# Optimization experiments

Measured on AMD Instinct MI355X. Metric: run time of the kernel, lower is better.

Reference implementation:

```python
import jax, jax.numpy as jnp
import numpy as np

VOCAB = 50000
D_EMB = 300
N_BINS = 11
B, LQ, LD = 64, 32, 1024
MU = np.array([1.0, 0.9, 0.7, 0.5, 0.3, 0.1, -0.1, -0.3, -0.5, -0.7, -0.9], dtype=np.float32)
SIGMA = np.array([1e-3] + [0.1] * 10, dtype=np.float32)


def setup_inputs() -> dict:
    key = jax.random.key(0)
    ks = jax.random.split(key, 8)
    inputs_q = jax.random.randint(ks[0], (B, LQ), 0, VOCAB, dtype=jnp.int64 if jax.config.jax_enable_x64 else jnp.int32)
    inputs_d = jax.random.randint(ks[1], (B, LD), 0, VOCAB, dtype=jnp.int64 if jax.config.jax_enable_x64 else jnp.int32)
    mask_q = jnp.ones((B, LQ), dtype=jnp.float32)
    mask_d = jnp.ones((B, LD), dtype=jnp.float32)
    word_emb = jax.random.normal(ks[2], (VOCAB, D_EMB), dtype=jnp.float32) * 0.1
    attn_table = jax.random.uniform(ks[3], (VOCAB, 1), dtype=jnp.float32)  # frozen IDF embedding
    idf_w = jax.random.normal(ks[4], (1, 1), dtype=jnp.float32)
    idf_b = jnp.zeros((1,), dtype=jnp.float32)
    dense_w = jax.random.normal(ks[5], (1, N_BINS), dtype=jnp.float32) * 0.1
    dense_b = jnp.zeros((1,), dtype=jnp.float32)
    return {
        'inputs_q': inputs_q, 'inputs_d': inputs_d,
        'mask_q': mask_q, 'mask_d': mask_d,
        'word_emb': word_emb, 'attn_table': attn_table,
        'idf_w': idf_w, 'idf_b': idf_b,
        'dense_w': dense_w, 'dense_b': dense_b,
    }


def _l2_normalize(x, eps=1e-12):
    # matches F.normalize(x, 2, dim=-1): x / max(||x||, eps)
    n = jnp.sqrt(jnp.sum(x * x, axis=-1, keepdims=True))
    return x / jnp.maximum(n, eps)


def reference(inputs_q, inputs_d, mask_q, mask_d, word_emb, attn_table,
              idf_w, idf_b, dense_w, dense_b):
    mu = jnp.asarray(MU)        # [K]
    sigma = jnp.asarray(SIGMA)  # [K]
    # idf attention on query tokens: Linear(1,1) on frozen embedding lookup
    attn_q = attn_table[inputs_q] * idf_w[0, 0] + idf_b[0]          # [B,Lq,1]
    q_embed = _l2_normalize(word_emb[inputs_q])                      # [B,Lq,E]
    d_embed = _l2_normalize(word_emb[inputs_d])                      # [B,Ld,E]
    sim = jnp.einsum('bqe,bde->bqd', q_embed, d_embed)               # [B,Lq,Ld]
    # RBF soft-histogram over n_bins kernels, doc tokens masked
    rbf = jnp.exp(-((sim[..., None] - mu) ** 2) / (sigma ** 2) / 2)  # [B,Lq,Ld,K]
    pooling_sum = jnp.einsum('bqdk,bd->bqk', rbf, mask_d)            # [B,Lq,K]
    wq = mask_q[..., None] * attn_q                                   # [B,Lq,1]
    log_pool = jnp.log(jnp.clip(pooling_sum, 1e-10)) * wq * 0.01     # [B,Lq,K]
    log_pooling_sum = jnp.sum(log_pool, axis=1)                      # [B,K]
    out = jnp.tanh(log_pooling_sum @ dense_w.T + dense_b)            # [B,1]
    return out[:, 0]                                                 # [B]
```

## Files before the change

kernel.cpp:

```cpp
#include <hip/hip_runtime.h>
#include <math.h>

#define VOCAB  50000
#define D_EMB  300
#define NBINS  11
#define BATCH  64
#define LQ     32
#define LD     1024
#define DTILE  64
#define NDT    (LD / DTILE)
#define NSTEP  10

typedef __attribute__((ext_vector_type(8))) short short8;
typedef __attribute__((ext_vector_type(4))) float floatx4;

__constant__ float c_mu[NBINS]  = {1.0f, 0.9f, 0.7f, 0.5f, 0.3f, 0.1f,
                                   -0.1f, -0.3f, -0.5f, -0.7f, -0.9f};
__constant__ float c_is2[NBINS] = {500000.0f, 50.f, 50.f, 50.f, 50.f, 50.f,
                                   50.f, 50.f, 50.f, 50.f, 50.f};

static __device__ __forceinline__ unsigned short f32_bf16(float f) {
  unsigned u = __float_as_uint(f);
  u += 0x7FFFu + ((u >> 16) & 1u);
  return (unsigned short)(u >> 16);
}
static __device__ __forceinline__ float bf16_f32(unsigned short h) {
  return __uint_as_float(((unsigned)h) << 16);
}

static __device__ __forceinline__ float stage_rows(
    const float* __restrict__ emb_row,
    short* __restrict__ region,
    int s_begin, int s_end, int khi, int lane)
{
  const float4* emb4 = (const float4*)emb_row;
  float p = 0.f;
  for (int s = s_begin; s < s_end; ++s) {
    const int k0 = 32 * s + 8 * khi;
    float4 fa = make_float4(0.f, 0.f, 0.f, 0.f);
    float4 fb = make_float4(0.f, 0.f, 0.f, 0.f);
    if (k0 < D_EMB)     fa = emb4[k0 >> 2];
    if (k0 + 4 < D_EMB) fb = emb4[(k0 >> 2) + 1];
    unsigned short h[8];
    h[0] = f32_bf16(fa.x); h[1] = f32_bf16(fa.y);
    h[2] = f32_bf16(fa.z); h[3] = f32_bf16(fa.w);
    h[4] = f32_bf16(fb.x); h[5] = f32_bf16(fb.y);
    h[6] = f32_bf16(fb.z); h[7] = f32_bf16(fb.w);
    short8 v;
#pragma unroll
    for (int j = 0; j < 8; ++j) {
      const float x = bf16_f32(h[j]);
      p += x * x;
      v[j] = (short)h[j];
    }
    *(short8*)(region + s * 512 + lane * 8) = v;
  }
  return p;
}

__global__ __launch_bounds__(256) void knrm_main(
    const int* __restrict__ inputs_q, const int* __restrict__ inputs_d,
    const float* __restrict__ mask_d, const float* __restrict__ word_emb,
    float* __restrict__ partial)
{
  const int b    = blockIdx.y;
  const int dt   = blockIdx.x;
  const int tid  = threadIdx.x;
  const int wid  = tid >> 6;
  const int lane = tid & 63;
  const int khi  = lane >> 4;
  const int rl   = lane & 15;

  __shared__ __align__(16) short Afrag[2 * NSTEP * 512];
  __shared__ __align__(16) short Bfrag[4 * NSTEP * 512];
  __shared__ float sumsq_s[96];
  __shared__ float invq_s[LQ], invd_s[DTILE], maskd_s[DTILE];
  __shared__ float red[4][16][NBINS];

  if (tid < 96) sumsq_s[tid] = 0.f;
  if (tid < DTILE) maskd_s[tid] = mask_d[b * LD + dt * DTILE + tid];
  __syncthreads();

  {
    int tok; float p;
    if (wid == 0) {
      tok = inputs_q[b * LQ + rl];
      p = stage_rows(word_emb + (size_t)tok * D_EMB, Afrag, 0, NSTEP, khi, lane);
      p += __shfl_xor(p, 16); p += __shfl_xor(p, 32);
      if (lane < 16) atomicAdd(&sumsq_s[lane], p);
      tok = inputs_d[b * LD + dt * DTILE + rl];
      p = stage_rows(word_emb + (size_t)tok * D_EMB, Bfrag, 0, 5, khi, lane);
      p += __shfl_xor(p, 16); p += __shfl_xor(p, 32);
      if (lane < 16) atomicAdd(&sumsq_s[32 + lane], p);
    } else if (wid == 1) {
      tok = inputs_q[b * LQ + 16 + rl];
      p = stage_rows(word_emb + (size_t)tok * D_EMB, Afrag + NSTEP * 512, 0, NSTEP, khi, lane);
      p += __shfl_xor(p, 16); p += __shfl_xor(p, 32);
      if (lane < 16) atomicAdd(&sumsq_s[16 + lane], p);
      tok = inputs_d[b * LD + dt * DTILE + rl];
      p = stage_rows(word_emb + (size_t)tok * D_EMB, Bfrag, 5, NSTEP, khi, lane);
      p += __shfl_xor(p, 16); p += __shfl_xor(p, 32);
      if (lane < 16) atomicAdd(&sumsq_s[32 + lane], p);
    } else if (wid == 2) {
      tok = inputs_d[b * LD + dt * DTILE + 16 + rl];
      p = stage_rows(word_emb + (size_t)tok * D_EMB, Bfrag + NSTEP * 512, 0, NSTEP, khi, lane);
      p += __shfl_xor(p, 16); p += __shfl_xor(p, 32);
      if (lane < 16) atomicAdd(&sumsq_s[48 + lane], p);
      tok = inputs_d[b * LD + dt * DTILE + 32 + rl];
      p = stage_rows(word_emb + (size_t)tok * D_EMB, Bfrag + 2 * NSTEP * 512, 0, 5, khi, lane);
      p += __shfl_xor(p, 16); p += __shfl_xor(p, 32);
      if (lane < 16) atomicAdd(&sumsq_s[64 + lane], p);
    } else {
      tok = inputs_d[b * LD + dt * DTILE + 48 + rl];
      p = stage_rows(word_emb + (size_t)tok * D_EMB, Bfrag + 3 * NSTEP * 512, 0, NSTEP, khi, lane);
      p += __shfl_xor(p, 16); p += __shfl_xor(p, 32);
      if (lane < 16) atomicAdd(&sumsq_s[80 + lane], p);
      tok = inputs_d[b * LD + dt * DTILE + 32 + rl];
      p = stage_rows(word_emb + (size_t)tok * D_EMB, Bfrag + 2 * NSTEP * 512, 5, NSTEP, khi, lane);
      p += __shfl_xor(p, 16); p += __shfl_xor(p, 32);
      if (lane < 16) atomicAdd(&sumsq_s[64 + lane], p);
    }
  }
  __syncthreads();

  if (tid < 96) {
    const float s   = sumsq_s[tid];
    const float inv = 1.f / fmaxf(sqrtf(s), 1e-12f);
    if (tid < 32) invq_s[tid] = inv; else invd_s[tid - 32] = inv;
  }
  __syncthreads();

  const int qt = wid >> 1, dp = wid & 1;
  const short* Ab = Afrag + qt * NSTEP * 512;
  const short* B0 = Bfrag + (2 * dp) * NSTEP * 512;
  const short* B1 = Bfrag + (2 * dp + 1) * NSTEP * 512;
  floatx4 acc0 = {0.f, 0.f, 0.f, 0.f};
  floatx4 acc1 = {0.f, 0.f, 0.f, 0.f};
#pragma unroll
  for (int s = 0; s < NSTEP; ++s) {
    const short8 a  = *(const short8*)(Ab + s * 512 + lane * 8);
    const short8 b0 = *(const short8*)(B0 + s * 512 + lane * 8);
    const short8 b1 = *(const short8*)(B1 + s * 512 + lane * 8);
    acc0 = __builtin_amdgcn_mfma_f32_16x16x32_bf16(a, b0, acc0, 0, 0, 0);
    acc1 = __builtin_amdgcn_mfma_f32_16x16x32_bf16(a, b1, acc1, 0, 0, 0);
  }

  float ps[4][NBINS];
#pragma unroll
  for (int r = 0; r < 4; ++r)
#pragma unroll
    for (int k = 0; k < NBINS; ++k) ps[r][k] = 0.f;

  float iq[4];
#pragma unroll
  for (int r = 0; r < 4; ++r) iq[r] = invq_s[16 * qt + 4 * khi + r];

#pragma unroll
  for (int t = 0; t < 2; ++t) {
    const int   dl = 32 * dp + 16 * t + rl;
    const float id = invd_s[dl];
    const float md = maskd_s[dl];
    const floatx4 acc = t ? acc1 : acc0;
#pragma unroll
    for (int r = 0; r < 4; ++r) {
      const float sv = acc[r] * iq[r] * id;
#pragma unroll
      for (int k = 0; k < NBINS; ++k) {
        const float d = sv - c_mu[k];
        ps[r][k] += md * __expf(-d * d * c_is2[k]);
      }
    }
  }

#pragma unroll
  for (int off = 1; off < 16; off <<= 1)
#pragma unroll
    for (int r = 0; r < 4; ++r)
#pragma unroll
      for (int k = 0; k < NBINS; ++k)
        ps[r][k] += __shfl_xor(ps[r][k], off);

  if (rl == 0)
#pragma unroll
    for (int r = 0; r < 4; ++r)
#pragma unroll
      for (int k = 0; k < NBINS; ++k)
        red[wid][4 * khi + r][k] = ps[r][k];
  __syncthreads();

  for (int v = tid; v < LQ * NBINS; v += 256) {
    const int q = v / NBINS, k = v % NBINS;
    const float sv = (q < 16) ? (red[0][q][k] + red[1][q][k])
                              : (red[2][q - 16][k] + red[3][q - 16][k]);
    partial[((size_t)(b * LQ + q) * NBINS + k) * NDT + dt] = sv;
  }
}

__global__ __launch_bounds__(128) void knrm_finalize(
    const float* __restrict__ partial, const int* __restrict__ inputs_q,
    const float* __restrict__ mask_q, const float* __restrict__ attn_table,
    const float* __restrict__ idf_w, const float* __restrict__ idf_b,
    const float* __restrict__ dense_w, const float* __restrict__ dense_b,
    float* __restrict__ out)
{
  const int b   = blockIdx.x;
  const int tid = threadIdx.x;
  __shared__ float pool[LQ][NBINS];
  __shared__ float wq_s[LQ];
  __shared__ float lps[NBINS];

  for (int v = tid; v < LQ * NBINS; v += 128) {
    const int q = v / NBINS, k = v % NBINS;
    const float* p = partial + ((size_t)(b * LQ + q) * NBINS + k) * NDT;
    float s = 0.f;
#pragma unroll
    for (int t = 0; t < NDT; ++t) s += p[t];
    pool[q][k] = logf(fmaxf(s, 1e-10f));
  }
  if (tid < LQ) {
    const int tok = inputs_q[b * LQ + tid];
    wq_s[tid] = mask_q[b * LQ + tid] * (attn_table[tok] * idf_w[0] + idf_b[0]);
  }
  __syncthreads();
  if (tid < NBINS) {
    float s = 0.f;
    for (int q = 0; q < LQ; ++q) s += pool[q][tid] * wq_s[q];
    lps[tid] = 0.01f * s;
  }
  __syncthreads();
  if (tid == 0) {
    float z = dense_b[0];
    for (int k = 0; k < NBINS; ++k) z += lps[k] * dense_w[k];
    out[b] = tanhf(z);
  }
}

extern "C" void kernel_launch(void* const* d_in, const int* in_sizes, int n_in,
                              void* d_out, int out_size, void* d_ws, size_t ws_size,
                              hipStream_t stream) {
  const int*   inputs_q  = (const int*)d_in[0];
  const int*   inputs_d  = (const int*)d_in[1];
  const float* mask_q    = (const float*)d_in[2];
  const float* mask_d    = (const float*)d_in[3];
  const float* word_emb  = (const float*)d_in[4];
  const float* attn_tab  = (const float*)d_in[5];
  const float* idf_w     = (const float*)d_in[6];
  const float* idf_b     = (const float*)d_in[7];
  const float* dense_w   = (const float*)d_in[8];
  const float* dense_b   = (const float*)d_in[9];
  float* out     = (float*)d_out;
  float* partial = (float*)d_ws;

  dim3 grid(NDT, BATCH);
  knrm_main<<<grid, 256, 0, stream>>>(inputs_q, inputs_d, mask_d, word_emb, partial);
  knrm_finalize<<<BATCH, 128, 0, stream>>>(partial, inputs_q, mask_q, attn_tab,
                                           idf_w, idf_b, dense_w, dense_b, out);
}
```

Before: 135.4 us.

## Precompute query bf16 fragments and norms once per batch in a prep kernel

Adds a knrm_prep kernel that gathers, converts and normalizes the query embeddings once per batch row and writes the MFMA A-fragments and inverse norms to workspace. The main kernel loads the A-fragments straight into registers instead of re-staging the query rows in every one of the 16 doc-tile blocks. Doc staging is rebalanced so each wave handles exactly one 16-row tile, which removes the shared atomics and one barrier. The cost is an extra kernel launch, a global round trip for the fragments, and more registers for the A operands.

Measured after the change: 138.4 us. +2.2%, slower.

```diff
diff --git a/kernel.cpp b/kernel.cpp
--- a/kernel.cpp
+++ b/kernel.cpp
@@ -10,6 +10,7 @@
 #define DTILE  64
 #define NDT    (LD / DTILE)
 #define NSTEP  10
+#define FRAG_BLOCK (NSTEP * 512)
 
 typedef __attribute__((ext_vector_type(8))) short short8;
 typedef __attribute__((ext_vector_type(4))) float floatx4;
@@ -31,11 +32,12 @@
 static __device__ __forceinline__ float stage_rows(
     const float* __restrict__ emb_row,
     short* __restrict__ region,
-    int s_begin, int s_end, int khi, int lane)
+    int khi, int lane)
 {
   const float4* emb4 = (const float4*)emb_row;
   float p = 0.f;
-  for (int s = s_begin; s < s_end; ++s) {
+#pragma unroll
+  for (int s = 0; s < NSTEP; ++s) {
     const int k0 = 32 * s + 8 * khi;
     float4 fa = make_float4(0.f, 0.f, 0.f, 0.f);
     float4 fb = make_float4(0.f, 0.f, 0.f, 0.f);
@@ -58,10 +60,25 @@
   return p;
 }
 
+__global__ __launch_bounds__(128) void knrm_prep(
+    const int* __restrict__ inputs_q, const float* __restrict__ word_emb,
+    short* __restrict__ afrag, float* __restrict__ invq)
+{
+  const int b    = blockIdx.x;
+  const int qt   = threadIdx.x >> 6;
+  const int lane = threadIdx.x & 63;
+  const int khi  = lane >> 4, rl = lane & 15;
+  const int tok  = inputs_q[b * LQ + 16 * qt + rl];
+  float p = stage_rows(word_emb + (size_t)tok * D_EMB,
+                       afrag + (size_t)(b * 2 + qt) * FRAG_BLOCK, khi, lane);
+  p += __shfl_xor(p, 16); p += __shfl_xor(p, 32);
+  if (lane < 16) invq[b * LQ + 16 * qt + lane] = 1.f / fmaxf(sqrtf(p), 1e-12f);
+}
+
 __global__ __launch_bounds__(256) void knrm_main(
-    const int* __restrict__ inputs_q, const int* __restrict__ inputs_d,
-    const float* __restrict__ mask_d, const float* __restrict__ word_emb,
-    float* __restrict__ partial)
+    const int* __restrict__ inputs_d, const float* __restrict__ mask_d,
+    const float* __restrict__ word_emb, const short* __restrict__ afrag,
+    const float* __restrict__ invq, float* __restrict__ partial)
 {
   const int b    = blockIdx.y;
   const int dt   = blockIdx.x;
@@ -70,79 +87,43 @@
   const int lane = tid & 63;
   const int khi  = lane >> 4;
   const int rl   = lane & 15;
-
-  __shared__ __align__(16) short Afrag[2 * NSTEP * 512];
-  __shared__ __align__(16) short Bfrag[4 * NSTEP * 512];
-  __shared__ float sumsq_s[96];
-  __shared__ float invq_s[LQ], invd_s[DTILE], maskd_s[DTILE];
+  const int qt   = wid >> 1;
+  const int dp   = wid & 1;
+
+  __shared__ __align__(16) short Bfrag[4 * FRAG_BLOCK];
+  __shared__ float invd_raw[DTILE];
+  __shared__ float maskd_s[DTILE];
   __shared__ float red[4][16][NBINS];
 
-  if (tid < 96) sumsq_s[tid] = 0.f;
+  short8 areg[NSTEP];
+  {
+    const short8* ag = (const short8*)(afrag + (size_t)(b * 2 + qt) * FRAG_BLOCK);
+#pragma unroll
+    for (int s = 0; s < NSTEP; ++s) areg[s] = ag[s * 64 + lane];
+  }
+  const float4 iq4 = *(const float4*)&invq[b * LQ + 16 * qt + 4 * khi];
+
   if (tid < DTILE) maskd_s[tid] = mask_d[b * LD + dt * DTILE + tid];
-  __syncthreads();
 
   {
-    int tok; float p;
-    if (wid == 0) {
-      tok = inputs_q[b * LQ + rl];
-      p = stage_rows(word_emb + (size_t)tok * D_EMB, Afrag, 0, NSTEP, khi, lane);
-      p += __shfl_xor(p, 16); p += __shfl_xor(p, 32);
-      if (lane < 16) atomicAdd(&sumsq_s[lane], p);
-      tok = inputs_d[b * LD + dt * DTILE + rl];
-      p = stage_rows(word_emb + (size_t)tok * D_EMB, Bfrag, 0, 5, khi, lane);
-      p += __shfl_xor(p, 16); p += __shfl_xor(p, 32);
-      if (lane < 16) atomicAdd(&sumsq_s[32 + lane], p);
-    } else if (wid == 1) {
-      tok = inputs_q[b * LQ + 16 + rl];
-      p = stage_rows(word_emb + (size_t)tok * D_EMB, Afrag + NSTEP * 512, 0, NSTEP, khi, lane);
-      p += __shfl_xor(p, 16); p += __shfl_xor(p, 32);
-      if (lane < 16) atomicAdd(&sumsq_s[16 + lane], p);
-      tok = inputs_d[b * LD + dt * DTILE + rl];
-      p = stage_rows(word_emb + (size_t)tok * D_EMB, Bfrag, 5, NSTEP, khi, lane);
-      p += __shfl_xor(p, 16); p += __shfl_xor(p, 32);
-      if (lane < 16) atomicAdd(&sumsq_s[32 + lane], p);
-    } else if (wid == 2) {
-      tok = inputs_d[b * LD + dt * DTILE + 16 + rl];
-      p = stage_rows(word_emb + (size_t)tok * D_EMB, Bfrag + NSTEP * 512, 0, NSTEP, khi, lane);
-      p += __shfl_xor(p, 16); p += __shfl_xor(p, 32);
-      if (lane < 16) atomicAdd(&sumsq_s[48 + lane], p);
-      tok = inputs_d[b * LD + dt * DTILE + 32 + rl];
-      p = stage_rows(word_emb + (size_t)tok * D_EMB, Bfrag + 2 * NSTEP * 512, 0, 5, khi, lane);
-      p += __shfl_xor(p, 16); p += __shfl_xor(p, 32);
-      if (lane < 16) atomicAdd(&sumsq_s[64 + lane], p);
-    } else {
-      tok = inputs_d[b * LD + dt * DTILE + 48 + rl];
-      p = stage_rows(word_emb + (size_t)tok * D_EMB, Bfrag + 3 * NSTEP * 512, 0, NSTEP, khi, lane);
-      p += __shfl_xor(p, 16); p += __shfl_xor(p, 32);
-      if (lane < 16) atomicAdd(&sumsq_s[80 + lane], p);
-      tok = inputs_d[b * LD + dt * DTILE + 32 + rl];
-      p = stage_rows(word_emb + (size_t)tok * D_EMB, Bfrag + 2 * NSTEP * 512, 5, NSTEP, khi, lane);
-      p += __shfl_xor(p, 16); p += __shfl_xor(p, 32);
-      if (lane < 16) atomicAdd(&sumsq_s[64 + lane], p);
-    }
-  }
-  __syncthreads();
-
-  if (tid < 96) {
-    const float s   = sumsq_s[tid];
-    const float inv = 1.f / fmaxf(sqrtf(s), 1e-12f);
-    if (tid < 32) invq_s[tid] = inv; else invd_s[tid - 32] = inv;
-  }
-  __syncthreads();
-
-  const int qt = wid >> 1, dp = wid & 1;
-  const short* Ab = Afrag + qt * NSTEP * 512;
-  const short* B0 = Bfrag + (2 * dp) * NSTEP * 512;
-  const short* B1 = Bfrag + (2 * dp + 1) * NSTEP * 512;
+    const int tok = inputs_d[b * LD + dt * DTILE + 16 * wid + rl];
+    float p = stage_rows(word_emb + (size_t)tok * D_EMB,
+                         Bfrag + wid * FRAG_BLOCK, khi, lane);
+    p += __shfl_xor(p, 16); p += __shfl_xor(p, 32);
+    if (lane < 16) invd_raw[16 * wid + lane] = p;
+  }
+  __syncthreads();
+
+  const short* B0 = Bfrag + (2 * dp) * FRAG_BLOCK;
+  const short* B1 = B0 + FRAG_BLOCK;
   floatx4 acc0 = {0.f, 0.f, 0.f, 0.f};
   floatx4 acc1 = {0.f, 0.f, 0.f, 0.f};
 #pragma unroll
   for (int s = 0; s < NSTEP; ++s) {
-    const short8 a  = *(const short8*)(Ab + s * 512 + lane * 8);
     const short8 b0 = *(const short8*)(B0 + s * 512 + lane * 8);
     const short8 b1 = *(const short8*)(B1 + s * 512 + lane * 8);
-    acc0 = __builtin_amdgcn_mfma_f32_16x16x32_bf16(a, b0, acc0, 0, 0, 0);
-    acc1 = __builtin_amdgcn_mfma_f32_16x16x32_bf16(a, b1, acc1, 0, 0, 0);
+    acc0 = __builtin_amdgcn_mfma_f32_16x16x32_bf16(areg[s], b0, acc0, 0, 0, 0);
+    acc1 = __builtin_amdgcn_mfma_f32_16x16x32_bf16(areg[s], b1, acc1, 0, 0, 0);
   }
 
   float ps[4][NBINS];
@@ -150,20 +131,16 @@
   for (int r = 0; r < 4; ++r)
 #pragma unroll
     for (int k = 0; k < NBINS; ++k) ps[r][k] = 0.f;
-
-  float iq[4];
-#pragma unroll
-  for (int r = 0; r < 4; ++r) iq[r] = invq_s[16 * qt + 4 * khi + r];
 
 #pragma unroll
   for (int t = 0; t < 2; ++t) {
     const int   dl = 32 * dp + 16 * t + rl;
-    const float id = invd_s[dl];
+    const float id = 1.f / fmaxf(sqrtf(invd_raw[dl]), 1e-12f);
     const float md = maskd_s[dl];
     const floatx4 acc = t ? acc1 : acc0;
 #pragma unroll
     for (int r = 0; r < 4; ++r) {
-      const float sv = acc[r] * iq[r] * id;
+      const float sv = acc[r] * iq4[r] * id;
 #pragma unroll
       for (int k = 0; k < NBINS; ++k) {
         const float d = sv - c_mu[k];
@@ -248,11 +225,16 @@
   const float* idf_b     = (const float*)d_in[7];
   const float* dense_w   = (const float*)d_in[8];
   const float* dense_b   = (const float*)d_in[9];
-  float* out     = (float*)d_out;
-  float* partial = (float*)d_ws;
-
+  float* out = (float*)d_out;
+
+  char*  ws      = (char*)d_ws;
+  float* partial = (float*)ws;
+  short* afrag   = (short*)(ws + (2u << 20));
+  float* invq    = (float*)(ws + (4u << 20));
+
+  knrm_prep<<<BATCH, 128, 0, stream>>>(inputs_q, word_emb, afrag, invq);
   dim3 grid(NDT, BATCH);
-  knrm_main<<<grid, 256, 0, stream>>>(inputs_q, inputs_d, mask_d, word_emb, partial);
+  knrm_main<<<grid, 256, 0, stream>>>(inputs_d, mask_d, word_emb, afrag, invq, partial);
   knrm_finalize<<<BATCH, 128, 0, stream>>>(partial, inputs_q, mask_q, attn_tab,
                                            idf_w, idf_b, dense_w, dense_b, out);
 }
```
